# Performance work log

Hardware: AMD Instinct MI355X
Metric: run time of the kernel (lower is better)

## Reference

```python
import jax, jax.numpy as jnp
import numpy as np

TEMPERATURE = 1.0  # spec.temperature, clamped to >=1e-6 in the original
NEG_INF = -1000000000.0


def setup_inputs() -> dict:
    key = jax.random.key(0)
    k_x, k_w1, k_b1, k_w2, k_b2 = jax.random.split(key, 5)
    N, d_in, d_h, E = 32768, 1024, 256, 64
    s1 = 1.0 / np.sqrt(d_in)
    s2 = 1.0 / np.sqrt(d_h)
    return {
        "stage_input": jax.random.normal(k_x, (N, d_in), dtype=jnp.float32),
        "w1": jax.random.uniform(k_w1, (d_in, d_h), jnp.float32, -s1, s1),
        "b1": jax.random.uniform(k_b1, (d_h,), jnp.float32, -s1, s1),
        "w2": jax.random.uniform(k_w2, (d_h, E), jnp.float32, -s2, s2),
        "b2": jax.random.uniform(k_b2, (E,), jnp.float32, -s2, s2),
        "top_k": 8,
    }


def reference(stage_input, w1, b1, w2, b2, top_k):
    # Router MLP: Linear -> ReLU -> (Dropout, eval=identity) -> Linear
    h = jax.nn.relu(stage_input @ w1 + b1)          # [N, d_hidden]
    logits = h @ w2 + b2                             # [N, E]

    scaled = logits / TEMPERATURE
    E = scaled.shape[-1]
    k = min(int(top_k), E)
    if 0 < k < E:
        vals, idx = jax.lax.top_k(scaled, k)         # [N, k]
        rows = jnp.arange(scaled.shape[0])[:, None]
        masked = jnp.full_like(scaled, NEG_INF).at[rows, idx].set(vals)
    else:
        masked = scaled

    probs = jax.nn.softmax(masked, axis=-1)          # [N, E]
    return logits, masked, probs
```

## Files before the change

kernel.cpp:

```cpp
#include <hip/hip_runtime.h>
#include <hip/hip_bf16.h>
#include <float.h>


#define N_ROWS 32768
#define D_IN   1024
#define D_H    256
#define N_E    64
#define NEG_INF_VAL (-1000000000.0f)

typedef _Float16 f16x8 __attribute__((ext_vector_type(8)));
typedef float    f32x4  __attribute__((ext_vector_type(4)));
typedef float    f32x16 __attribute__((ext_vector_type(16)));

__global__ __launch_bounds__(256) void split_weights_kernel(
    const float* __restrict__ w1, const float* __restrict__ w2,
    _Float16* __restrict__ w1pk_h, _Float16* __restrict__ w1pk_l,
    _Float16* __restrict__ w2hT, _Float16* __restrict__ w2lT) {
  int idx = blockIdx.x * 256 + threadIdx.x;
  if (idx < D_IN * D_H) {
    const int k = idx >> 8;
    const int n = idx & 255;
    const float v = w1[idx];
    const _Float16 hi = (_Float16)v;
    const _Float16 lo = (_Float16)(v - (float)hi);
    const int wv = n >> 6, nf = (n >> 5) & 1, l31 = n & 31;
    const int it = k >> 6, kf = (k >> 4) & 3, kg = (k >> 3) & 1, j = k & 7;
    const int lane = kg * 32 + l31;
    const int off = ((((wv * 16 + it) * 4 + kf) * 2 + nf) * 64 + lane) * 8 + j;
    w1pk_h[off] = hi;
    w1pk_l[off] = lo;
  } else {
    idx -= D_IN * D_H;
    const int k = idx >> 6;
    const int e = idx & 63;
    const float v = w2[idx];
    const _Float16 hi = (_Float16)v;
    const _Float16 lo = (_Float16)(v - (float)hi);
    w2hT[e * D_H + k] = hi;
    w2lT[e * D_H + k] = lo;
  }
}

__global__ __launch_bounds__(256, 2) void gemm1_mfma_kernel(
    const float* __restrict__ x, const _Float16* __restrict__ w1pk_h,
    const _Float16* __restrict__ w1pk_l, const float* __restrict__ b1,
    float* __restrict__ h) {
  __shared__ char lds[32768];

  const int t  = threadIdx.x;
  const int m0 = blockIdx.x * 64;

  const int srow = t >> 2;
  const int skb2 = (t & 3) * 32;
  const int sw   = (srow & 7) << 4;

  const int wv   = t >> 6;
  const int lane = t & 63;
  const int l31  = lane & 31;
  const int kg   = lane >> 5;

  const float* xrowp = x + (size_t)(m0 + srow) * D_IN + (t & 3) * 16;
  const f16x8* bph = (const f16x8*)w1pk_h;
  const f16x8* bpl = (const f16x8*)w1pk_l;

  f32x16 acc[2][2];
#pragma unroll
  for (int i = 0; i < 16; ++i) {
    acc[0][0][i] = 0.f; acc[0][1][i] = 0.f;
    acc[1][0][i] = 0.f; acc[1][1][i] = 0.f;
  }

  f16x8 uh00, uh01, uh10, uh11, uh20, uh21, uh30, uh31;
  f16x8 ul00, ul01, ul10, ul11, ul20, ul21, ul30, ul31;
  f16x8 vh00, vh01, vh10, vh11, vh20, vh21, vh30, vh31;
  f16x8 vl00, vl01, vl10, vl11, vl20, vl21, vl30, vl31;

#define STAGE_WRITE(bufi, q0, q1, q2, q3)                                    \
  do {                                                                       \
    const float vv[16] = {q0.x, q0.y, q0.z, q0.w, q1.x, q1.y, q1.z, q1.w,    \
                          q2.x, q2.y, q2.z, q2.w, q3.x, q3.y, q3.z, q3.w};   \
    f16x8 hi0, hi1, lo0, lo1;                                                \
    _Pragma("unroll") for (int j = 0; j < 8; ++j) {                          \
      const _Float16 hv = (_Float16)vv[j];                                   \
      hi0[j] = hv; lo0[j] = (_Float16)(vv[j] - (float)hv);                   \
    }                                                                        \
    _Pragma("unroll") for (int j = 0; j < 8; ++j) {                          \
      const _Float16 hv = (_Float16)vv[8 + j];                               \
      hi1[j] = hv; lo1[j] = (_Float16)(vv[8 + j] - (float)hv);               \
    }                                                                        \
    char* bb = lds + (bufi) * 16384 + srow * 256;                            \
    *(f16x8*)(bb + ((skb2 + 0) ^ sw)) = hi0;                                 \
    *(f16x8*)(bb + ((skb2 + 16) ^ sw)) = hi1;                                \
    *(f16x8*)(bb + 128 + ((skb2 + 0) ^ sw)) = lo0;                           \
    *(f16x8*)(bb + 128 + ((skb2 + 16) ^ sw)) = lo1;                          \
  } while (0)

#define LOAD_B(BH, BL, itv)                                                  \
  do {                                                                       \
    const int ch = (wv * 16 + (itv)) * 512 + lane;                           \
    BH##00 = bph[ch + 0 * 64]; BH##01 = bph[ch + 1 * 64];                    \
    BH##10 = bph[ch + 2 * 64]; BH##11 = bph[ch + 3 * 64];                    \
    BH##20 = bph[ch + 4 * 64]; BH##21 = bph[ch + 5 * 64];                    \
    BH##30 = bph[ch + 6 * 64]; BH##31 = bph[ch + 7 * 64];                    \
    BL##00 = bpl[ch + 0 * 64]; BL##01 = bpl[ch + 1 * 64];                    \
    BL##10 = bpl[ch + 2 * 64]; BL##11 = bpl[ch + 3 * 64];                    \
    BL##20 = bpl[ch + 4 * 64]; BL##21 = bpl[ch + 5 * 64];                    \
    BL##30 = bpl[ch + 6 * 64]; BL##31 = bpl[ch + 7 * 64];                    \
  } while (0)

#define MFMA_KF(rb, kfv, BH0, BL0, BH1, BL1)                                 \
  do {                                                                       \
    const int kb = (kfv) * 32 + kg * 16;                                     \
    _Pragma("unroll") for (int mf = 0; mf < 2; ++mf) {                       \
      const int ra = mf * 32 + l31;                                          \
      const char* ap = (rb) + ra * 256 + (kb ^ ((ra & 7) << 4));             \
      const f16x8 ah = *(const f16x8*)(ap);                                  \
      const f16x8 al = *(const f16x8*)(ap + 128);                            \
      acc[mf][0] = __builtin_amdgcn_mfma_f32_32x32x16_f16(al, BH0, acc[mf][0], 0, 0, 0); \
      acc[mf][0] = __builtin_amdgcn_mfma_f32_32x32x16_f16(ah, BL0, acc[mf][0], 0, 0, 0); \
      acc[mf][0] = __builtin_amdgcn_mfma_f32_32x32x16_f16(ah, BH0, acc[mf][0], 0, 0, 0); \
      acc[mf][1] = __builtin_amdgcn_mfma_f32_32x32x16_f16(al, BH1, acc[mf][1], 0, 0, 0); \
      acc[mf][1] = __builtin_amdgcn_mfma_f32_32x32x16_f16(ah, BL1, acc[mf][1], 0, 0, 0); \
      acc[mf][1] = __builtin_amdgcn_mfma_f32_32x32x16_f16(ah, BH1, acc[mf][1], 0, 0, 0); \
    }                                                                        \
  } while (0)

#define GSTEP(ITV, LB, CH, CL, NH, NL)                                       \
  do {                                                                       \
    float4 p0, p1, p2, p3;                                                   \
    const bool more = (ITV) + 1 < 16;                                        \
    if (more) {                                                              \
      const float4* xp = (const float4*)(xrowp + ((ITV) + 1) * 64);          \
      p0 = xp[0]; p1 = xp[1]; p2 = xp[2]; p3 = xp[3];                        \
      LOAD_B(NH, NL, (ITV) + 1);                                             \
    }                                                                        \
    const char* rb = lds + (LB) * 16384;                                     \
    MFMA_KF(rb, 0, CH##00, CL##00, CH##01, CL##01);                          \
    MFMA_KF(rb, 1, CH##10, CL##10, CH##11, CL##11);                          \
    MFMA_KF(rb, 2, CH##20, CL##20, CH##21, CL##21);                          \
    MFMA_KF(rb, 3, CH##30, CL##30, CH##31, CL##31);                          \
    if (more) STAGE_WRITE(1 - (LB), p0, p1, p2, p3);                         \
    __syncthreads();                                                         \
  } while (0)

  {
    const float4* xp = (const float4*)(xrowp);
    const float4 q0 = xp[0], q1 = xp[1], q2 = xp[2], q3 = xp[3];
    STAGE_WRITE(0, q0, q1, q2, q3);
    LOAD_B(uh, ul, 0);
  }
  __syncthreads();

  for (int ii = 0; ii < 8; ++ii) {
    GSTEP(2 * ii,     0, uh, ul, vh, vl);
    GSTEP(2 * ii + 1, 1, vh, vl, uh, ul);
  }

#pragma unroll
  for (int nf = 0; nf < 2; ++nf) {
    const int colg = wv * 64 + nf * 32 + l31;
    const float bias = b1[colg];
#pragma unroll
    for (int mf = 0; mf < 2; ++mf) {
#pragma unroll
      for (int r = 0; r < 16; ++r) {
        const int row = (r & 3) + 8 * (r >> 2) + 4 * kg;
        const int mg = m0 + mf * 32 + row;
        h[(size_t)mg * D_H + colg] = fmaxf(acc[mf][nf][r] + bias, 0.0f);
      }
    }
  }
#undef GSTEP
#undef MFMA_KF
#undef LOAD_B
#undef STAGE_WRITE
}

__global__ __launch_bounds__(256) void router_mfma_kernel(
    const float* __restrict__ h, const _Float16* __restrict__ w2hT,
    const _Float16* __restrict__ w2lT, const float* __restrict__ b2,
    const int* __restrict__ topk_p, float* __restrict__ out_logits,
    float* __restrict__ out_masked, float* __restrict__ out_probs) {
  const int t    = threadIdx.x;
  const int wid  = t >> 6;
  const int lane = t & 63;
  const int c    = lane & 15;
  const int kg   = lane >> 4;

  const int rowbase = blockIdx.x * 64 + wid * 16;

  f32x4 acc0 = {0.f, 0.f, 0.f, 0.f};
  f32x4 acc1 = {0.f, 0.f, 0.f, 0.f};
  f32x4 acc2 = {0.f, 0.f, 0.f, 0.f};
  f32x4 acc3 = {0.f, 0.f, 0.f, 0.f};

  const float*    hp  = h    + (size_t)(rowbase + c) * D_H + kg * 8;
  const _Float16* bhp = w2hT + c * D_H + kg * 8;
  const _Float16* blp = w2lT + c * D_H + kg * 8;

#pragma unroll
  for (int s = 0; s < 8; ++s) {
    const float4 a0 = *(const float4*)(hp + s * 32);
    const float4 a1 = *(const float4*)(hp + s * 32 + 4);
    const float av[8] = {a0.x, a0.y, a0.z, a0.w, a1.x, a1.y, a1.z, a1.w};
    f16x8 ah, al;
#pragma unroll
    for (int j = 0; j < 8; ++j) {
      const _Float16 hv = (_Float16)av[j];
      ah[j] = hv;
      al[j] = (_Float16)(av[j] - (float)hv);
    }
    const f16x8 bh0 = *(const f16x8*)(bhp + 0 * 16 * D_H + s * 32);
    const f16x8 bl0 = *(const f16x8*)(blp + 0 * 16 * D_H + s * 32);
    const f16x8 bh1 = *(const f16x8*)(bhp + 1 * 16 * D_H + s * 32);
    const f16x8 bl1 = *(const f16x8*)(blp + 1 * 16 * D_H + s * 32);
    const f16x8 bh2 = *(const f16x8*)(bhp + 2 * 16 * D_H + s * 32);
    const f16x8 bl2 = *(const f16x8*)(blp + 2 * 16 * D_H + s * 32);
    const f16x8 bh3 = *(const f16x8*)(bhp + 3 * 16 * D_H + s * 32);
    const f16x8 bl3 = *(const f16x8*)(blp + 3 * 16 * D_H + s * 32);
    acc0 = __builtin_amdgcn_mfma_f32_16x16x32_f16(al, bh0, acc0, 0, 0, 0);
    acc0 = __builtin_amdgcn_mfma_f32_16x16x32_f16(ah, bl0, acc0, 0, 0, 0);
    acc0 = __builtin_amdgcn_mfma_f32_16x16x32_f16(ah, bh0, acc0, 0, 0, 0);
    acc1 = __builtin_amdgcn_mfma_f32_16x16x32_f16(al, bh1, acc1, 0, 0, 0);
    acc1 = __builtin_amdgcn_mfma_f32_16x16x32_f16(ah, bl1, acc1, 0, 0, 0);
    acc1 = __builtin_amdgcn_mfma_f32_16x16x32_f16(ah, bh1, acc1, 0, 0, 0);
    acc2 = __builtin_amdgcn_mfma_f32_16x16x32_f16(al, bh2, acc2, 0, 0, 0);
    acc2 = __builtin_amdgcn_mfma_f32_16x16x32_f16(ah, bl2, acc2, 0, 0, 0);
    acc2 = __builtin_amdgcn_mfma_f32_16x16x32_f16(ah, bh2, acc2, 0, 0, 0);
    acc3 = __builtin_amdgcn_mfma_f32_16x16x32_f16(al, bh3, acc3, 0, 0, 0);
    acc3 = __builtin_amdgcn_mfma_f32_16x16x32_f16(ah, bl3, acc3, 0, 0, 0);
    acc3 = __builtin_amdgcn_mfma_f32_16x16x32_f16(ah, bh3, acc3, 0, 0, 0);
  }

  const int K = topk_p[0];
  const bool doMask = (K > 0 && K < N_E);
  const float b2v0 = b2[c], b2v1 = b2[16 + c], b2v2 = b2[32 + c],
              b2v3 = b2[48 + c];

#pragma unroll
  for (int r = 0; r < 4; ++r) {
    const int row = rowbase + kg * 4 + r;
    float* lg = out_logits + (size_t)row * N_E;
    float* mk = out_masked + (size_t)row * N_E;
    float* pb = out_probs  + (size_t)row * N_E;

    const float v0 = acc0[r] + b2v0;
    const float v1 = acc1[r] + b2v1;
    const float v2 = acc2[r] + b2v2;
    const float v3 = acc3[r] + b2v3;
    lg[c] = v0; lg[16 + c] = v1; lg[32 + c] = v2; lg[48 + c] = v3;

    bool s0 = true, s1 = true, s2 = true, s3 = true;
    if (doMask) {
      s0 = s1 = s2 = s3 = false;
      float c0 = v0, c1 = v1, c2 = v2, c3 = v3;
      for (int it = 0; it < K; ++it) {
        float m = c0; int mi = c;
        if (c1 > m) { m = c1; mi = 16 + c; }
        if (c2 > m) { m = c2; mi = 32 + c; }
        if (c3 > m) { m = c3; mi = 48 + c; }
#pragma unroll
        for (int off = 1; off <= 8; off <<= 1) {
          const float om = __shfl_xor(m, off);
          const int   oi = __shfl_xor(mi, off);
          if (om > m || (om == m && oi < mi)) { m = om; mi = oi; }
        }
        if ((mi & 15) == c) {
          const int f = mi >> 4;
          s0 = s0 || (f == 0); c0 = (f == 0) ? -FLT_MAX : c0;
          s1 = s1 || (f == 1); c1 = (f == 1) ? -FLT_MAX : c1;
          s2 = s2 || (f == 2); c2 = (f == 2) ? -FLT_MAX : c2;
          s3 = s3 || (f == 3); c3 = (f == 3) ? -FLT_MAX : c3;
        }
      }
    }
    const float m0 = s0 ? v0 : NEG_INF_VAL;
    const float m1 = s1 ? v1 : NEG_INF_VAL;
    const float m2 = s2 ? v2 : NEG_INF_VAL;
    const float m3 = s3 ? v3 : NEG_INF_VAL;
    mk[c] = m0; mk[16 + c] = m1; mk[32 + c] = m2; mk[48 + c] = m3;

    float mx = fmaxf(fmaxf(m0, m1), fmaxf(m2, m3));
#pragma unroll
    for (int off = 1; off <= 8; off <<= 1) mx = fmaxf(mx, __shfl_xor(mx, off));
    const float e0 = __expf(m0 - mx);
    const float e1 = __expf(m1 - mx);
    const float e2 = __expf(m2 - mx);
    const float e3 = __expf(m3 - mx);
    float sm = e0 + e1 + e2 + e3;
#pragma unroll
    for (int off = 1; off <= 8; off <<= 1) sm += __shfl_xor(sm, off);
    const float inv = 1.0f / sm;
    pb[c] = e0 * inv; pb[16 + c] = e1 * inv; pb[32 + c] = e2 * inv;
    pb[48 + c] = e3 * inv;
  }
}

extern "C" void kernel_launch(void* const* d_in, const int* in_sizes, int n_in,
                              void* d_out, int out_size, void* d_ws,
                              size_t ws_size, hipStream_t stream) {
  const float* x  = (const float*)d_in[0];
  const float* w1 = (const float*)d_in[1];
  const float* b1 = (const float*)d_in[2];
  const float* w2 = (const float*)d_in[3];
  const float* b2 = (const float*)d_in[4];
  const int* topk = (const int*)d_in[5];

  char* ws = (char*)d_ws;
  _Float16* w1pk_h = (_Float16*)(ws);
  _Float16* w1pk_l = (_Float16*)(ws + 524288);
  _Float16* w2hT   = (_Float16*)(ws + 1048576);
  _Float16* w2lT   = (_Float16*)(ws + 1081344);
  float*    hbuf   = (float*)(ws + 1114112);

  float* out_logits = (float*)d_out;
  float* out_masked = out_logits + (size_t)N_ROWS * N_E;
  float* out_probs  = out_masked + (size_t)N_ROWS * N_E;

  split_weights_kernel<<<(D_IN * D_H + D_H * N_E) / 256, 256, 0, stream>>>(
      w1, w2, w1pk_h, w1pk_l, w2hT, w2lT);

  gemm1_mfma_kernel<<<N_ROWS / 64, 256, 0, stream>>>(x, w1pk_h, w1pk_l, b1,
                                                     hbuf);

  router_mfma_kernel<<<N_ROWS / 64, 256, 0, stream>>>(
      hbuf, w2hT, w2lT, b2, topk, out_logits, out_masked, out_probs);
}
```

Before: 102.4 us.

## Fuse GEMM1 and router epilogue into one kernel with LDS-resident hidden

Merges the first GEMM and the router/top-k/softmax kernel into a single kernel. The hidden activations are split into fp16 hi/lo halves in LDS instead of going through a global fp32 buffer, and W2 is pre-packed into an MFMA-friendly layout. This removes the hidden-state round trip through memory and one launch. It also deepens x prefetch to two steps ahead and reorders the MFMAs to interleave independent accumulators. LDS doubles to 64KB, which may limit occupancy to fewer blocks per CU.

```diff
diff --git a/kernel.cpp b/kernel.cpp
--- a/kernel.cpp
+++ b/kernel.cpp
@@ -13,10 +13,13 @@
 typedef float    f32x4  __attribute__((ext_vector_type(4)));
 typedef float    f32x16 __attribute__((ext_vector_type(16)));
 
+#define MM32(A, B, C) __builtin_amdgcn_mfma_f32_32x32x16_f16(A, B, C, 0, 0, 0)
+#define MM16(A, B, C) __builtin_amdgcn_mfma_f32_16x16x32_f16(A, B, C, 0, 0, 0)
+
 __global__ __launch_bounds__(256) void split_weights_kernel(
     const float* __restrict__ w1, const float* __restrict__ w2,
     _Float16* __restrict__ w1pk_h, _Float16* __restrict__ w1pk_l,
-    _Float16* __restrict__ w2hT, _Float16* __restrict__ w2lT) {
+    _Float16* __restrict__ w2pk_h, _Float16* __restrict__ w2pk_l) {
   int idx = blockIdx.x * 256 + threadIdx.x;
   if (idx < D_IN * D_H) {
     const int k = idx >> 8;
@@ -37,16 +40,23 @@
     const float v = w2[idx];
     const _Float16 hi = (_Float16)v;
     const _Float16 lo = (_Float16)(v - (float)hi);
-    w2hT[e * D_H + k] = hi;
-    w2lT[e * D_H + k] = lo;
+    const int s = k >> 5, kg = (k >> 3) & 3, j = k & 7;
+    const int f = e >> 4, cc = e & 15;
+    const int lane = kg * 16 + cc;
+    const int off = ((s * 4 + f) * 64 + lane) * 8 + j;
+    w2pk_h[off] = hi;
+    w2pk_l[off] = lo;
   }
 }
 
-__global__ __launch_bounds__(256, 2) void gemm1_mfma_kernel(
+__global__ __launch_bounds__(256, 2) void fused_router_kernel(
     const float* __restrict__ x, const _Float16* __restrict__ w1pk_h,
     const _Float16* __restrict__ w1pk_l, const float* __restrict__ b1,
-    float* __restrict__ h) {
-  __shared__ char lds[32768];
+    const _Float16* __restrict__ w2pk_h, const _Float16* __restrict__ w2pk_l,
+    const float* __restrict__ b2, const int* __restrict__ topk_p,
+    float* __restrict__ out_logits, float* __restrict__ out_masked,
+    float* __restrict__ out_probs) {
+  __shared__ char lds[65536];
 
   const int t  = threadIdx.x;
   const int m0 = blockIdx.x * 64;
@@ -64,17 +74,17 @@
   const f16x8* bph = (const f16x8*)w1pk_h;
   const f16x8* bpl = (const f16x8*)w1pk_l;
 
-  f32x16 acc[2][2];
+  f32x16 acc00, acc01, acc10, acc11;
 #pragma unroll
   for (int i = 0; i < 16; ++i) {
-    acc[0][0][i] = 0.f; acc[0][1][i] = 0.f;
-    acc[1][0][i] = 0.f; acc[1][1][i] = 0.f;
+    acc00[i] = 0.f; acc01[i] = 0.f; acc10[i] = 0.f; acc11[i] = 0.f;
   }
 
   f16x8 uh00, uh01, uh10, uh11, uh20, uh21, uh30, uh31;
   f16x8 ul00, ul01, ul10, ul11, ul20, ul21, ul30, ul31;
   f16x8 vh00, vh01, vh10, vh11, vh20, vh21, vh30, vh31;
   f16x8 vl00, vl01, vl10, vl11, vl20, vl21, vl30, vl31;
+  float4 sa0, sa1, sa2, sa3, sb0, sb1, sb2, sb3;
 
 #define STAGE_WRITE(bufi, q0, q1, q2, q3)                                    \
   do {                                                                       \
@@ -112,35 +122,33 @@
 #define MFMA_KF(rb, kfv, BH0, BL0, BH1, BL1)                                 \
   do {                                                                       \
     const int kb = (kfv) * 32 + kg * 16;                                     \
-    _Pragma("unroll") for (int mf = 0; mf < 2; ++mf) {                       \
-      const int ra = mf * 32 + l31;                                          \
-      const char* ap = (rb) + ra * 256 + (kb ^ ((ra & 7) << 4));             \
-      const f16x8 ah = *(const f16x8*)(ap);                                  \
-      const f16x8 al = *(const f16x8*)(ap + 128);                            \
-      acc[mf][0] = __builtin_amdgcn_mfma_f32_32x32x16_f16(al, BH0, acc[mf][0], 0, 0, 0); \
-      acc[mf][0] = __builtin_amdgcn_mfma_f32_32x32x16_f16(ah, BL0, acc[mf][0], 0, 0, 0); \
-      acc[mf][0] = __builtin_amdgcn_mfma_f32_32x32x16_f16(ah, BH0, acc[mf][0], 0, 0, 0); \
-      acc[mf][1] = __builtin_amdgcn_mfma_f32_32x32x16_f16(al, BH1, acc[mf][1], 0, 0, 0); \
-      acc[mf][1] = __builtin_amdgcn_mfma_f32_32x32x16_f16(ah, BL1, acc[mf][1], 0, 0, 0); \
-      acc[mf][1] = __builtin_amdgcn_mfma_f32_32x32x16_f16(ah, BH1, acc[mf][1], 0, 0, 0); \
+    const char* ap0 = (rb) + l31 * 256 + (kb ^ ((l31 & 7) << 4));            \
+    const char* ap1 = ap0 + 32 * 256;                                        \
+    const f16x8 ah0 = *(const f16x8*)(ap0);                                  \
+    const f16x8 al0 = *(const f16x8*)(ap0 + 128);                            \
+    const f16x8 ah1 = *(const f16x8*)(ap1);                                  \
+    const f16x8 al1 = *(const f16x8*)(ap1 + 128);                            \
+    acc00 = MM32(al0, BH0, acc00); acc01 = MM32(al0, BH1, acc01);            \
+    acc10 = MM32(al1, BH0, acc10); acc11 = MM32(al1, BH1, acc11);            \
+    acc00 = MM32(ah0, BL0, acc00); acc01 = MM32(ah0, BL1, acc01);            \
+    acc10 = MM32(ah1, BL0, acc10); acc11 = MM32(ah1, BL1, acc11);            \
+    acc00 = MM32(ah0, BH0, acc00); acc01 = MM32(ah0, BH1, acc01);            \
+    acc10 = MM32(ah1, BH0, acc10); acc11 = MM32(ah1, BH1, acc11);            \
+  } while (0)
+
+#define GSTEP(ITV, LB, CH, CL, NH, NL, SL, SS)                               \
+  do {                                                                       \
+    if ((ITV) + 2 < 16) {                                                    \
+      const float4* xp = (const float4*)(xrowp + ((ITV) + 2) * 64);          \
+      SL##0 = xp[0]; SL##1 = xp[1]; SL##2 = xp[2]; SL##3 = xp[3];            \
     }                                                                        \
-  } while (0)
-
-#define GSTEP(ITV, LB, CH, CL, NH, NL)                                       \
-  do {                                                                       \
-    float4 p0, p1, p2, p3;                                                   \
-    const bool more = (ITV) + 1 < 16;                                        \
-    if (more) {                                                              \
-      const float4* xp = (const float4*)(xrowp + ((ITV) + 1) * 64);          \
-      p0 = xp[0]; p1 = xp[1]; p2 = xp[2]; p3 = xp[3];                        \
-      LOAD_B(NH, NL, (ITV) + 1);                                             \
-    }                                                                        \
+    if ((ITV) + 1 < 16) LOAD_B(NH, NL, (ITV) + 1);                           \
     const char* rb = lds + (LB) * 16384;                                     \
     MFMA_KF(rb, 0, CH##00, CL##00, CH##01, CL##01);                          \
     MFMA_KF(rb, 1, CH##10, CL##10, CH##11, CL##11);                          \
     MFMA_KF(rb, 2, CH##20, CL##20, CH##21, CL##21);                          \
     MFMA_KF(rb, 3, CH##30, CL##30, CH##31, CL##31);                          \
-    if (more) STAGE_WRITE(1 - (LB), p0, p1, p2, p3);                         \
+    if ((ITV) + 1 < 16) STAGE_WRITE(1 - (LB), SS##0, SS##1, SS##2, SS##3);   \
     __syncthreads();                                                         \
   } while (0)
 
@@ -148,107 +156,86 @@
     const float4* xp = (const float4*)(xrowp);
     const float4 q0 = xp[0], q1 = xp[1], q2 = xp[2], q3 = xp[3];
     STAGE_WRITE(0, q0, q1, q2, q3);
+    const float4* xp1 = (const float4*)(xrowp + 64);
+    sb0 = xp1[0]; sb1 = xp1[1]; sb2 = xp1[2]; sb3 = xp1[3];
     LOAD_B(uh, ul, 0);
   }
   __syncthreads();
 
+#pragma unroll
   for (int ii = 0; ii < 8; ++ii) {
-    GSTEP(2 * ii,     0, uh, ul, vh, vl);
-    GSTEP(2 * ii + 1, 1, vh, vl, uh, ul);
-  }
-
-#pragma unroll
-  for (int nf = 0; nf < 2; ++nf) {
-    const int colg = wv * 64 + nf * 32 + l31;
-    const float bias = b1[colg];
-#pragma unroll
-    for (int mf = 0; mf < 2; ++mf) {
-#pragma unroll
-      for (int r = 0; r < 16; ++r) {
-        const int row = (r & 3) + 8 * (r >> 2) + 4 * kg;
-        const int mg = m0 + mf * 32 + row;
-        h[(size_t)mg * D_H + colg] = fmaxf(acc[mf][nf][r] + bias, 0.0f);
-      }
-    }
-  }
-#undef GSTEP
-#undef MFMA_KF
-#undef LOAD_B
-#undef STAGE_WRITE
-}
-
-__global__ __launch_bounds__(256) void router_mfma_kernel(
-    const float* __restrict__ h, const _Float16* __restrict__ w2hT,
-    const _Float16* __restrict__ w2lT, const float* __restrict__ b2,
-    const int* __restrict__ topk_p, float* __restrict__ out_logits,
-    float* __restrict__ out_masked, float* __restrict__ out_probs) {
-  const int t    = threadIdx.x;
-  const int wid  = t >> 6;
-  const int lane = t & 63;
-  const int c    = lane & 15;
-  const int kg   = lane >> 4;
-
-  const int rowbase = blockIdx.x * 64 + wid * 16;
-
-  f32x4 acc0 = {0.f, 0.f, 0.f, 0.f};
-  f32x4 acc1 = {0.f, 0.f, 0.f, 0.f};
-  f32x4 acc2 = {0.f, 0.f, 0.f, 0.f};
-  f32x4 acc3 = {0.f, 0.f, 0.f, 0.f};
-
-  const float*    hp  = h    + (size_t)(rowbase + c) * D_H + kg * 8;
-  const _Float16* bhp = w2hT + c * D_H + kg * 8;
-  const _Float16* blp = w2lT + c * D_H + kg * 8;
+    GSTEP(2 * ii,     0, uh, ul, vh, vl, sa, sb);
+    GSTEP(2 * ii + 1, 1, vh, vl, uh, ul, sb, sa);
+  }
+
+#define EPI(ACC, MF, NF)                                                     \
+  do {                                                                       \
+    const int colg = wv * 64 + (NF) * 32 + l31;                              \
+    const float bias = b1[colg];                                             \
+    _Pragma("unroll") for (int r = 0; r < 16; ++r) {                         \
+      const int row = (MF) * 32 + (r & 3) + 8 * (r >> 2) + 4 * kg;           \
+      const float hv = fmaxf(ACC[r] + bias, 0.0f);                           \
+      const _Float16 hhi = (_Float16)hv;                                     \
+      const _Float16 hlo = (_Float16)(hv - (float)hhi);                      \
+      const int byo = row * 512 + ((colg * 2) ^ ((row & 7) << 4));           \
+      *(_Float16*)(lds + byo) = hhi;                                         \
+      *(_Float16*)(lds + 32768 + byo) = hlo;                                 \
+    }                                                                        \
+  } while (0)
+
+  EPI(acc00, 0, 0); EPI(acc01, 0, 1); EPI(acc10, 1, 0); EPI(acc11, 1, 1);
+#undef EPI
+  __syncthreads();
+
+  const int c   = lane & 15;
+  const int kg4 = lane >> 4;
+  const int rowl = wv * 16 + c;
+  const int sw2 = (rowl & 7) << 4;
+  const char* hhb = lds + rowl * 512;
+  const char* hlb = lds + 32768 + rowl * 512;
+  const f16x8* b2ph = (const f16x8*)w2pk_h;
+  const f16x8* b2pl = (const f16x8*)w2pk_l;
+
+  f32x4 r0 = {0.f, 0.f, 0.f, 0.f};
+  f32x4 r1 = {0.f, 0.f, 0.f, 0.f};
+  f32x4 r2 = {0.f, 0.f, 0.f, 0.f};
+  f32x4 r3 = {0.f, 0.f, 0.f, 0.f};
 
 #pragma unroll
   for (int s = 0; s < 8; ++s) {
-    const float4 a0 = *(const float4*)(hp + s * 32);
-    const float4 a1 = *(const float4*)(hp + s * 32 + 4);
-    const float av[8] = {a0.x, a0.y, a0.z, a0.w, a1.x, a1.y, a1.z, a1.w};
-    f16x8 ah, al;
-#pragma unroll
-    for (int j = 0; j < 8; ++j) {
-      const _Float16 hv = (_Float16)av[j];
-      ah[j] = hv;
-      al[j] = (_Float16)(av[j] - (float)hv);
-    }
-    const f16x8 bh0 = *(const f16x8*)(bhp + 0 * 16 * D_H + s * 32);
-    const f16x8 bl0 = *(const f16x8*)(blp + 0 * 16 * D_H + s * 32);
-    const f16x8 bh1 = *(const f16x8*)(bhp + 1 * 16 * D_H + s * 32);
-    const f16x8 bl1 = *(const f16x8*)(blp + 1 * 16 * D_H + s * 32);
-    const f16x8 bh2 = *(const f16x8*)(bhp + 2 * 16 * D_H + s * 32);
-    const f16x8 bl2 = *(const f16x8*)(blp + 2 * 16 * D_H + s * 32);
-    const f16x8 bh3 = *(const f16x8*)(bhp + 3 * 16 * D_H + s * 32);
-    const f16x8 bl3 = *(const f16x8*)(blp + 3 * 16 * D_H + s * 32);
-    acc0 = __builtin_amdgcn_mfma_f32_16x16x32_f16(al, bh0, acc0, 0, 0, 0);
-    acc0 = __builtin_amdgcn_mfma_f32_16x16x32_f16(ah, bl0, acc0, 0, 0, 0);
-    acc0 = __builtin_amdgcn_mfma_f32_16x16x32_f16(ah, bh0, acc0, 0, 0, 0);
-    acc1 = __builtin_amdgcn_mfma_f32_16x16x32_f16(al, bh1, acc1, 0, 0, 0);
-    acc1 = __builtin_amdgcn_mfma_f32_16x16x32_f16(ah, bl1, acc1, 0, 0, 0);
-    acc1 = __builtin_amdgcn_mfma_f32_16x16x32_f16(ah, bh1, acc1, 0, 0, 0);
-    acc2 = __builtin_amdgcn_mfma_f32_16x16x32_f16(al, bh2, acc2, 0, 0, 0);
-    acc2 = __builtin_amdgcn_mfma_f32_16x16x32_f16(ah, bl2, acc2, 0, 0, 0);
-    acc2 = __builtin_amdgcn_mfma_f32_16x16x32_f16(ah, bh2, acc2, 0, 0, 0);
-    acc3 = __builtin_amdgcn_mfma_f32_16x16x32_f16(al, bh3, acc3, 0, 0, 0);
-    acc3 = __builtin_amdgcn_mfma_f32_16x16x32_f16(ah, bl3, acc3, 0, 0, 0);
-    acc3 = __builtin_amdgcn_mfma_f32_16x16x32_f16(ah, bh3, acc3, 0, 0, 0);
+    const int kb = (s * 64 + kg4 * 16) ^ sw2;
+    const f16x8 ah = *(const f16x8*)(hhb + kb);
+    const f16x8 al = *(const f16x8*)(hlb + kb);
+    const int ch = s * 256 + lane;
+    const f16x8 bh0 = b2ph[ch +   0], bh1 = b2ph[ch +  64];
+    const f16x8 bh2 = b2ph[ch + 128], bh3 = b2ph[ch + 192];
+    const f16x8 bl0 = b2pl[ch +   0], bl1 = b2pl[ch +  64];
+    const f16x8 bl2 = b2pl[ch + 128], bl3 = b2pl[ch + 192];
+    r0 = MM16(al, bh0, r0); r1 = MM16(al, bh1, r1);
+    r2 = MM16(al, bh2, r2); r3 = MM16(al, bh3, r3);
+    r0 = MM16(ah, bl0, r0); r1 = MM16(ah, bl1, r1);
+    r2 = MM16(ah, bl2, r2); r3 = MM16(ah, bl3, r3);
+    r0 = MM16(ah, bh0, r0); r1 = MM16(ah, bh1, r1);
+    r2 = MM16(ah, bh2, r2); r3 = MM16(ah, bh3, r3);
   }
 
   const int K = topk_p[0];
   const bool doMask = (K > 0 && K < N_E);
   const float b2v0 = b2[c], b2v1 = b2[16 + c], b2v2 = b2[32 + c],
               b2v3 = b2[48 + c];
+  const int rowbase = m0 + wv * 16;
 
 #pragma unroll
   for (int r = 0; r < 4; ++r) {
-    const int row = rowbase + kg * 4 + r;
+    const int row = rowbase + kg4 * 4 + r;
     float* lg = out_logits + (size_t)row * N_E;
     float* mk = out_masked + (size_t)row * N_E;
     float* pb = out_probs  + (size_t)row * N_E;
 
-    const float v0 = acc0[r] + b2v0;
-    const float v1 = acc1[r] + b2v1;
-    const float v2 = acc2[r] + b2v2;
-    const float v3 = acc3[r] + b2v3;
+    const float v0 = r0[r] + b2v0;
+    const float v1 = r1[r] + b2v1;
+    const float v2 = r2[r] + b2v2;
+    const float v3 = r3[r] + b2v3;
     lg[c] = v0; lg[16 + c] = v1; lg[32 + c] = v2; lg[48 + c] = v3;
 
     bool s0 = true, s1 = true, s2 = true, s3 = true;
@@ -275,19 +262,19 @@
         }
       }
     }
-    const float m0 = s0 ? v0 : NEG_INF_VAL;
-    const float m1 = s1 ? v1 : NEG_INF_VAL;
-    const float m2 = s2 ? v2 : NEG_INF_VAL;
-    const float m3 = s3 ? v3 : NEG_INF_VAL;
-    mk[c] = m0; mk[16 + c] = m1; mk[32 + c] = m2; mk[48 + c] = m3;
-
-    float mx = fmaxf(fmaxf(m0, m1), fmaxf(m2, m3));
+    const float m0v = s0 ? v0 : NEG_INF_VAL;
+    const float m1v = s1 ? v1 : NEG_INF_VAL;
+    const float m2v = s2 ? v2 : NEG_INF_VAL;
+    const float m3v = s3 ? v3 : NEG_INF_VAL;
+    mk[c] = m0v; mk[16 + c] = m1v; mk[32 + c] = m2v; mk[48 + c] = m3v;
+
+    float mx = fmaxf(fmaxf(m0v, m1v), fmaxf(m2v, m3v));
 #pragma unroll
     for (int off = 1; off <= 8; off <<= 1) mx = fmaxf(mx, __shfl_xor(mx, off));
-    const float e0 = __expf(m0 - mx);
-    const float e1 = __expf(m1 - mx);
-    const float e2 = __expf(m2 - mx);
-    const float e3 = __expf(m3 - mx);
+    const float e0 = __expf(m0v - mx);
+    const float e1 = __expf(m1v - mx);
+    const float e2 = __expf(m2v - mx);
+    const float e3 = __expf(m3v - mx);
     float sm = e0 + e1 + e2 + e3;
 #pragma unroll
     for (int off = 1; off <= 8; off <<= 1) sm += __shfl_xor(sm, off);
@@ -295,6 +282,10 @@
     pb[c] = e0 * inv; pb[16 + c] = e1 * inv; pb[32 + c] = e2 * inv;
     pb[48 + c] = e3 * inv;
   }
+#undef GSTEP
+#undef MFMA_KF
+#undef LOAD_B
+#undef STAGE_WRITE
 }
 
 extern "C" void kernel_launch(void* const* d_in, const int* in_sizes, int n_in,
@@ -310,20 +301,17 @@
   char* ws = (char*)d_ws;
   _Float16* w1pk_h = (_Float16*)(ws);
   _Float16* w1pk_l = (_Float16*)(ws + 524288);
-  _Float16* w2hT   = (_Float16*)(ws + 1048576);
-  _Float16* w2lT   = (_Float16*)(ws + 1081344);
-  float*    hbuf   = (float*)(ws + 1114112);
+  _Float16* w2pk_h = (_Float16*)(ws + 1048576);
+  _Float16* w2pk_l = (_Float16*)(ws + 1081344);
 
   float* out_logits = (float*)d_out;
   float* out_masked = out_logits + (size_t)N_ROWS * N_E;
   float* out_probs  = out_masked + (size_t)N_ROWS * N_E;
 
   split_weights_kernel<<<(D_IN * D_H + D_H * N_E) / 256, 256, 0, stream>>>(
-      w1, w2, w1pk_h, w1pk_l, w2hT, w2lT);
-
-  gemm1_mfma_kernel<<<N_ROWS / 64, 256, 0, stream>>>(x, w1pk_h, w1pk_l, b1,
-                                                     hbuf);
-
-  router_mfma_kernel<<<N_ROWS / 64, 256, 0, stream>>>(
-      hbuf, w2hT, w2lT, b2, topk, out_logits, out_masked, out_probs);
+      w1, w2, w1pk_h, w1pk_l, w2pk_h, w2pk_l);
+
+  fused_router_kernel<<<N_ROWS / 64, 256, 0, stream>>>(
+      x, w1pk_h, w1pk_l, b1, w2pk_h, w2pk_l, b2, topk, out_logits, out_masked,
+      out_probs);
 }
```

Result: faster. 81.89 us (-20.0%).
